# Performance work log

Hardware: AMD Instinct MI355X
Metric: run time of the kernel (lower is better)

Reference implementation:

```python
import jax, jax.numpy as jnp
import numpy as np

NEG_INF = -9e15
LEAKY_SLOPE = 0.01  # PyTorch F.leaky_relu default


def setup_inputs() -> dict:
    key = jax.random.key(0)
    k1, k2, k3, k4 = jax.random.split(key, 4)
    B, N, Fin, Fout = 4, 4096, 64, 64
    X = jax.random.normal(k1, (B, N, Fin), dtype=jnp.float32)
    A = jax.random.randint(k2, (N, N), 0, 2, dtype=jnp.int32)
    weight = jax.random.normal(k3, (Fin, Fout), dtype=jnp.float32) * 0.15
    a = jax.random.normal(k4, (2 * Fout, 1), dtype=jnp.float32) * 0.15
    return {"X": X, "A": A, "weight": weight, "a": a}


def reference(X, A, weight, a):
    B, N, _ = X.shape
    Fout = weight.shape[1]
    # add self loops: A[i,i] = 1
    mask = (A > 0) | jnp.eye(N, dtype=bool)  # [N, N]
    Xw = jnp.matmul(X, weight)  # [B, N, Fout]
    # additive attention: e_ij = leaky_relu(a_l . x_i + a_r . x_j)
    # equivalent to the repeat/cat/matmul in the original, without O(N^2 F) memory
    a_l = a[:Fout, 0]   # [Fout]
    a_r = a[Fout:, 0]   # [Fout]
    left = jnp.einsum('bnf,f->bn', Xw, a_l)   # [B, N]
    right = jnp.einsum('bnf,f->bn', Xw, a_r)  # [B, N]
    e = left[:, :, None] + right[:, None, :]  # [B, N, N]
    e = jnp.where(e >= 0, e, LEAKY_SLOPE * e)
    att = jnp.where(mask[None, :, :], e, NEG_INF)
    att = jax.nn.softmax(att, axis=-1)  # dropout p=0 -> identity
    out = jnp.matmul(att, Xw)  # [B, N, Fout]
    return out
```

## Files before the change

### kernel.cpp

```cpp
#include <hip/hip_runtime.h>
#include <hip/hip_bf16.h>
#include <math.h>

#define BB 4
#define NN 4096
#define FF 64
#define KS (NN / 32)
#define NKW (KS / 4)
#define C0F 3.35462628e-4f
#define C1F 3.35462628e-6f

typedef _Float16 half8 __attribute__((ext_vector_type(8)));
typedef float f32x4 __attribute__((ext_vector_type(4)));

__global__ void k_pack(const int* __restrict__ A, unsigned int* __restrict__ bitsT) {
    int idx = blockIdx.x * 256 + threadIdx.x;
    int row = idx >> 12;
    int col = idx & (NN - 1);
    bool pred = (A[idx] > 0) || (row == col);
    unsigned long long m = __ballot(pred);
    int lane = threadIdx.x & 63;
    if (lane == 0)  bitsT[(size_t)(col >> 5) * NN + row] = (unsigned int)(m & 0xffffffffULL);
    if (lane == 32) bitsT[(size_t)(col >> 5) * NN + row] = (unsigned int)(m >> 32);
}

__global__ __launch_bounds__(256, 2)
void k_pre(const float* __restrict__ X, const float* __restrict__ W,
           const float* __restrict__ avec, _Float16* __restrict__ XwP,
           float2* __restrict__ LE, float2* __restrict__ RE) {
    __shared__ __align__(16) float Wl[64 * 64];
    __shared__ __align__(16) float Xl[32][64];
    __shared__ __align__(16) float T[32][65];
    __shared__ float al[64];
    __shared__ float ar[64];
    const int t = threadIdx.x;
    const int lane = t & 63;
    const int wv = t >> 6;
    const int r0 = blockIdx.x * 32;

    #pragma unroll
    for (int k = 0; k < 16; ++k) Wl[t + k * 256] = W[t + k * 256];
    if (t < 64) { al[t] = avec[t]; ar[t] = avec[64 + t]; }
    {
        const float4* xs = (const float4*)(X + (size_t)r0 * 64);
        float4* xd = (float4*)&Xl[0][0];
        xd[t] = xs[t];
        xd[t + 256] = xs[t + 256];
    }
    __syncthreads();

    float Wreg[64];
    #pragma unroll
    for (int k = 0; k < 64; ++k) Wreg[k] = Wl[k * 64 + lane];

    #pragma unroll
    for (int rr = 0; rr < 8; ++rr) {
        int lrow = wv * 8 + rr;
        int row  = r0 + lrow;
        float a0 = 0.f, a1 = 0.f, a2 = 0.f, a3 = 0.f;
        #pragma unroll
        for (int k = 0; k < 64; k += 4) {
            float4 x = *(const float4*)&Xl[lrow][k];
            a0 = fmaf(x.x, Wreg[k],     a0);
            a1 = fmaf(x.y, Wreg[k + 1], a1);
            a2 = fmaf(x.z, Wreg[k + 2], a2);
            a3 = fmaf(x.w, Wreg[k + 3], a3);
        }
        float acc = (a0 + a1) + (a2 + a3);
        T[lrow][lane] = acc;

        float lv = acc * al[lane];
        float rv = acc * ar[lane];
        #pragma unroll
        for (int off = 32; off; off >>= 1) {
            lv += __shfl_xor(lv, off, 64);
            rv += __shfl_xor(rv, off, 64);
        }
        if (lane == 0) {
            LE[row] = make_float2(lv, __expf(lv - 8.f));
            RE[row] = make_float2(rv, __expf(rv));
        }
    }
    __syncthreads();

    int b  = r0 >> 12;
    int ks = (r0 & (NN - 1)) >> 5;
    int ct = t >> 6;
    int q  = lane >> 4, n = lane & 15;
    half8 h;
    #pragma unroll
    for (int jj = 0; jj < 8; ++jj)
        h[jj] = (_Float16)T[q * 8 + jj][ct * 16 + n];
    *(half8*)&XwP[((((size_t)b * KS + ks) * 4 + ct) * 64 + lane) * 8] = h;
}

__global__ __launch_bounds__(256, 4)
void k_main(const _Float16* __restrict__ XwP, const float2* __restrict__ LE,
            const float2* __restrict__ RE, const unsigned int* __restrict__ bitsT,
            float* __restrict__ out) {
    __shared__ __align__(16) char smem[32768];
    float2* REs = (float2*)smem;
    float (*Lacc)[16][68] = (float (*)[16][68])smem;
    float* Lsum = (float*)(smem + 8704);

    const int t  = threadIdx.x;
    const int b  = blockIdx.y;
    const int i0 = blockIdx.x * 16;

    const int lane = t & 63;
    const int wv   = t >> 6;
    const int lm   = lane & 15;
    const int q    = lane >> 4;

    const int row0 = i0 + lm;
    const float2 le0 = LE[b * NN + row0];
    const _Float16* xp = XwP + (size_t)b * KS * 2048 + (size_t)lane * 8;

    {
        const float4* rsrc = (const float4*)(RE + (size_t)b * NN);
        float4* rdst = (float4*)REs;
        #pragma unroll
        for (int k = 0; k < 8; ++k) rdst[t + k * 256] = rsrc[t + k * 256];
    }
    __syncthreads();

    f32x4 acc[4];
    f32x4 sacc = (f32x4)0.f;
    #pragma unroll
    for (int ct = 0; ct < 4; ++ct) acc[ct] = (f32x4)0.f;
    half8 vones;
    #pragma unroll
    for (int k = 0; k < 8; ++k) vones[k] = (_Float16)1.0f;

    const int ks0 = wv * NKW;

    const _Float16* base = xp + (size_t)ks0 * 2048;
    half8 nb0 = *(const half8*)(base + 0 * 512);
    half8 nb1 = *(const half8*)(base + 1 * 512);
    half8 nb2 = *(const half8*)(base + 2 * 512);
    half8 nb3 = *(const half8*)(base + 3 * 512);
    unsigned int nw0 = bitsT[(size_t)ks0 * NN + row0];

    #pragma unroll 4
    for (int kk = 0; kk < NKW; ++kk) {
        half8 bf0 = nb0, bf1 = nb1, bf2 = nb2, bf3 = nb3;
        unsigned int w0 = nw0 >> (q * 8);

        {
            int nk = kk + 1 < NKW ? kk + 1 : kk;
            const _Float16* nbase = xp + (size_t)(ks0 + nk) * 2048;
            nb0 = *(const half8*)(nbase + 0 * 512);
            nb1 = *(const half8*)(nbase + 1 * 512);
            nb2 = *(const half8*)(nbase + 2 * 512);
            nb3 = *(const half8*)(nbase + 3 * 512);
            nw0 = bitsT[(size_t)(ks0 + nk) * NN + row0];
        }

        const float4* rp = (const float4*)(REs + (ks0 + kk) * 32 + q * 8);
        float4 ra = rp[0], rb = rp[1], rc = rp[2], rd = rp[3];
        float r8[8]  = {ra.x, ra.z, rb.x, rb.z, rc.x, rc.z, rd.x, rd.z};
        float er8[8] = {ra.y, ra.w, rb.y, rb.w, rc.y, rc.w, rd.y, rd.w};

        half8 a0;
        #pragma unroll
        for (int jj = 0; jj < 8; ++jj) {
            float e0 = le0.x + r8[jj];
            float p0 = fmaxf(le0.y * er8[jj], fmaf(e0, C1F, C0F));
            p0 = ((w0 >> jj) & 1u) ? p0 : 0.f;
            a0[jj] = (_Float16)p0;
        }

        acc[0] = __builtin_amdgcn_mfma_f32_16x16x32_f16(a0, bf0, acc[0], 0, 0, 0);
        acc[1] = __builtin_amdgcn_mfma_f32_16x16x32_f16(a0, bf1, acc[1], 0, 0, 0);
        acc[2] = __builtin_amdgcn_mfma_f32_16x16x32_f16(a0, bf2, acc[2], 0, 0, 0);
        acc[3] = __builtin_amdgcn_mfma_f32_16x16x32_f16(a0, bf3, acc[3], 0, 0, 0);
        sacc   = __builtin_amdgcn_mfma_f32_16x16x32_f16(a0, vones, sacc, 0, 0, 0);
    }

    __syncthreads();

    if (wv >= 2) {
        #pragma unroll
        for (int r = 0; r < 4; ++r) {
            int lrow = q * 4 + r;
            #pragma unroll
            for (int ct = 0; ct < 4; ++ct)
                Lacc[wv - 2][lrow][ct * 16 + lm] = acc[ct][r];
            if (lm == 0) Lsum[(wv - 2) * 16 + lrow] = sacc[r];
        }
    }
    __syncthreads();
    if (wv < 2) {
        #pragma unroll
        for (int r = 0; r < 4; ++r) {
            int lrow = q * 4 + r;
            #pragma unroll
            for (int ct = 0; ct < 4; ++ct)
                Lacc[wv][lrow][ct * 16 + lm] += acc[ct][r];
            if (lm == 0) Lsum[wv * 16 + lrow] += sacc[r];
        }
    }
    __syncthreads();
    {
        int lrow = t >> 4;
        int c0   = (t & 15) * 4;
        float s = Lsum[0 * 16 + lrow] + Lsum[1 * 16 + lrow];
        float inv = 1.f / s;
        float4 o;
        o.x = (Lacc[0][lrow][c0 + 0] + Lacc[1][lrow][c0 + 0]) * inv;
        o.y = (Lacc[0][lrow][c0 + 1] + Lacc[1][lrow][c0 + 1]) * inv;
        o.z = (Lacc[0][lrow][c0 + 2] + Lacc[1][lrow][c0 + 2]) * inv;
        o.w = (Lacc[0][lrow][c0 + 3] + Lacc[1][lrow][c0 + 3]) * inv;
        *(float4*)&out[((size_t)(b * NN + i0 + lrow) << 6) + c0] = o;
    }
}

extern "C" void kernel_launch(void* const* d_in, const int* in_sizes, int n_in,
                              void* d_out, int out_size, void* d_ws, size_t ws_size,
                              hipStream_t stream) {
    const float* X    = (const float*)d_in[0];
    const int*   A    = (const int*)d_in[1];
    const float* W    = (const float*)d_in[2];
    const float* avec = (const float*)d_in[3];
    float* out = (float*)d_out;

    char* ws = (char*)d_ws;
    size_t off = 0;
    _Float16* XwP = (_Float16*)(ws + off); off += (size_t)BB * NN * FF * 2;
    float2* LE = (float2*)(ws + off);      off += (size_t)BB * NN * 8;
    float2* RE = (float2*)(ws + off);      off += (size_t)BB * NN * 8;
    unsigned int* bitsT = (unsigned int*)(ws + off);
    off += (size_t)KS * NN * 4;
    (void)off; (void)ws_size;

    k_pack<<<NN * NN / 256, 256, 0, stream>>>(A, bitsT);
    k_pre<<<BB * NN / 32, 256, 0, stream>>>(X, W, avec, XwP, LE, RE);
    k_main<<<dim3(NN / 16, BB), 256, 0, stream>>>(XwP, LE, RE, bitsT, out);
}
```

Baseline: 153.5 us.

## Process two 16-row tiles per block to reuse Xw fragments and RE loads

Each k_main block now handles 32 query rows instead of 16, computing two sets of attention weights and MFMA accumulators against the same loaded Xw fragments and shared RE values. This halves the grid and the global traffic for the XwP value matrix per output row, and it amortizes the RE shared-memory staging. In exchange it raises register pressure, so launch bounds drop to 2 blocks/SM and the unroll to 2, and fewer blocks (512) may leave the GPU less occupied.

Result: faster. 147.4 us (-3.9%).

```diff
diff --git a/kernel.cpp b/kernel.cpp
--- a/kernel.cpp
+++ b/kernel.cpp
@@ -94,26 +94,28 @@
     *(half8*)&XwP[((((size_t)b * KS + ks) * 4 + ct) * 64 + lane) * 8] = h;
 }
 
-__global__ __launch_bounds__(256, 4)
+__global__ __launch_bounds__(256, 2)
 void k_main(const _Float16* __restrict__ XwP, const float2* __restrict__ LE,
             const float2* __restrict__ RE, const unsigned int* __restrict__ bitsT,
             float* __restrict__ out) {
     __shared__ __align__(16) char smem[32768];
     float2* REs = (float2*)smem;
-    float (*Lacc)[16][68] = (float (*)[16][68])smem;
-    float* Lsum = (float*)(smem + 8704);
+    float (*Lacc)[32][68] = (float (*)[32][68])smem;
+    float* Lsum = (float*)(smem + 17408);
 
     const int t  = threadIdx.x;
     const int b  = blockIdx.y;
-    const int i0 = blockIdx.x * 16;
+    const int i0 = blockIdx.x * 32;
 
     const int lane = t & 63;
     const int wv   = t >> 6;
     const int lm   = lane & 15;
     const int q    = lane >> 4;
 
-    const int row0 = i0 + lm;
-    const float2 le0 = LE[b * NN + row0];
+    const int rowa = i0 + lm;
+    const int rowb = i0 + 16 + lm;
+    const float2 lea = LE[b * NN + rowa];
+    const float2 leb = LE[b * NN + rowb];
     const _Float16* xp = XwP + (size_t)b * KS * 2048 + (size_t)lane * 8;
 
     {
@@ -124,10 +126,10 @@
     }
     __syncthreads();
 
-    f32x4 acc[4];
-    f32x4 sacc = (f32x4)0.f;
-    #pragma unroll
-    for (int ct = 0; ct < 4; ++ct) acc[ct] = (f32x4)0.f;
+    f32x4 acca[4], accb[4];
+    f32x4 sacca = (f32x4)0.f, saccb = (f32x4)0.f;
+    #pragma unroll
+    for (int ct = 0; ct < 4; ++ct) { acca[ct] = (f32x4)0.f; accb[ct] = (f32x4)0.f; }
     half8 vones;
     #pragma unroll
     for (int k = 0; k < 8; ++k) vones[k] = (_Float16)1.0f;
@@ -139,12 +141,14 @@
     half8 nb1 = *(const half8*)(base + 1 * 512);
     half8 nb2 = *(const half8*)(base + 2 * 512);
     half8 nb3 = *(const half8*)(base + 3 * 512);
-    unsigned int nw0 = bitsT[(size_t)ks0 * NN + row0];
-
-    #pragma unroll 4
+    unsigned int nwa = bitsT[(size_t)ks0 * NN + rowa];
+    unsigned int nwb = bitsT[(size_t)ks0 * NN + rowb];
+
+    #pragma unroll 2
     for (int kk = 0; kk < NKW; ++kk) {
         half8 bf0 = nb0, bf1 = nb1, bf2 = nb2, bf3 = nb3;
-        unsigned int w0 = nw0 >> (q * 8);
+        unsigned int wa = nwa >> (q * 8);
+        unsigned int wb = nwb >> (q * 8);
 
         {
             int nk = kk + 1 < NKW ? kk + 1 : kk;
@@ -153,7 +157,8 @@
             nb1 = *(const half8*)(nbase + 1 * 512);
             nb2 = *(const half8*)(nbase + 2 * 512);
             nb3 = *(const half8*)(nbase + 3 * 512);
-            nw0 = bitsT[(size_t)(ks0 + nk) * NN + row0];
+            nwa = bitsT[(size_t)(ks0 + nk) * NN + rowa];
+            nwb = bitsT[(size_t)(ks0 + nk) * NN + rowb];
         }
 
         const float4* rp = (const float4*)(REs + (ks0 + kk) * 32 + q * 8);
@@ -161,20 +166,32 @@
         float r8[8]  = {ra.x, ra.z, rb.x, rb.z, rc.x, rc.z, rd.x, rd.z};
         float er8[8] = {ra.y, ra.w, rb.y, rb.w, rc.y, rc.w, rd.y, rd.w};
 
-        half8 a0;
+        half8 a0a, a0b;
         #pragma unroll
         for (int jj = 0; jj < 8; ++jj) {
-            float e0 = le0.x + r8[jj];
-            float p0 = fmaxf(le0.y * er8[jj], fmaf(e0, C1F, C0F));
-            p0 = ((w0 >> jj) & 1u) ? p0 : 0.f;
-            a0[jj] = (_Float16)p0;
-        }
-
-        acc[0] = __builtin_amdgcn_mfma_f32_16x16x32_f16(a0, bf0, acc[0], 0, 0, 0);
-        acc[1] = __builtin_amdgcn_mfma_f32_16x16x32_f16(a0, bf1, acc[1], 0, 0, 0);
-        acc[2] = __builtin_amdgcn_mfma_f32_16x16x32_f16(a0, bf2, acc[2], 0, 0, 0);
-        acc[3] = __builtin_amdgcn_mfma_f32_16x16x32_f16(a0, bf3, acc[3], 0, 0, 0);
-        sacc   = __builtin_amdgcn_mfma_f32_16x16x32_f16(a0, vones, sacc, 0, 0, 0);
+            float e0 = lea.x + r8[jj];
+            float p0 = fmaxf(lea.y * er8[jj], fmaf(e0, C1F, C0F));
+            p0 = ((wa >> jj) & 1u) ? p0 : 0.f;
+            a0a[jj] = (_Float16)p0;
+        }
+        acca[0] = __builtin_amdgcn_mfma_f32_16x16x32_f16(a0a, bf0, acca[0], 0, 0, 0);
+        acca[1] = __builtin_amdgcn_mfma_f32_16x16x32_f16(a0a, bf1, acca[1], 0, 0, 0);
+        acca[2] = __builtin_amdgcn_mfma_f32_16x16x32_f16(a0a, bf2, acca[2], 0, 0, 0);
+        acca[3] = __builtin_amdgcn_mfma_f32_16x16x32_f16(a0a, bf3, acca[3], 0, 0, 0);
+        sacca   = __builtin_amdgcn_mfma_f32_16x16x32_f16(a0a, vones, sacca, 0, 0, 0);
+
+        #pragma unroll
+        for (int jj = 0; jj < 8; ++jj) {
+            float e0 = leb.x + r8[jj];
+            float p0 = fmaxf(leb.y * er8[jj], fmaf(e0, C1F, C0F));
+            p0 = ((wb >> jj) & 1u) ? p0 : 0.f;
+            a0b[jj] = (_Float16)p0;
+        }
+        accb[0] = __builtin_amdgcn_mfma_f32_16x16x32_f16(a0b, bf0, accb[0], 0, 0, 0);
+        accb[1] = __builtin_amdgcn_mfma_f32_16x16x32_f16(a0b, bf1, accb[1], 0, 0, 0);
+        accb[2] = __builtin_amdgcn_mfma_f32_16x16x32_f16(a0b, bf2, accb[2], 0, 0, 0);
+        accb[3] = __builtin_amdgcn_mfma_f32_16x16x32_f16(a0b, bf3, accb[3], 0, 0, 0);
+        saccb   = __builtin_amdgcn_mfma_f32_16x16x32_f16(a0b, vones, saccb, 0, 0, 0);
     }
 
     __syncthreads();
@@ -184,9 +201,14 @@
         for (int r = 0; r < 4; ++r) {
             int lrow = q * 4 + r;
             #pragma unroll
-            for (int ct = 0; ct < 4; ++ct)
-                Lacc[wv - 2][lrow][ct * 16 + lm] = acc[ct][r];
-            if (lm == 0) Lsum[(wv - 2) * 16 + lrow] = sacc[r];
+            for (int ct = 0; ct < 4; ++ct) {
+                Lacc[wv - 2][lrow][ct * 16 + lm]      = acca[ct][r];
+                Lacc[wv - 2][16 + lrow][ct * 16 + lm] = accb[ct][r];
+            }
+            if (lm == 0) {
+                Lsum[(wv - 2) * 32 + lrow]      = sacca[r];
+                Lsum[(wv - 2) * 32 + 16 + lrow] = saccb[r];
+            }
         }
     }
     __syncthreads();
@@ -195,16 +217,23 @@
         for (int r = 0; r < 4; ++r) {
             int lrow = q * 4 + r;
             #pragma unroll
-            for (int ct = 0; ct < 4; ++ct)
-                Lacc[wv][lrow][ct * 16 + lm] += acc[ct][r];
-            if (lm == 0) Lsum[wv * 16 + lrow] += sacc[r];
-        }
-    }
-    __syncthreads();
-    {
-        int lrow = t >> 4;
-        int c0   = (t & 15) * 4;
-        float s = Lsum[0 * 16 + lrow] + Lsum[1 * 16 + lrow];
+            for (int ct = 0; ct < 4; ++ct) {
+                Lacc[wv][lrow][ct * 16 + lm]      += acca[ct][r];
+                Lacc[wv][16 + lrow][ct * 16 + lm] += accb[ct][r];
+            }
+            if (lm == 0) {
+                Lsum[wv * 32 + lrow]      += sacca[r];
+                Lsum[wv * 32 + 16 + lrow] += saccb[r];
+            }
+        }
+    }
+    __syncthreads();
+    #pragma unroll
+    for (int it = 0; it < 2; ++it) {
+        int idx  = t + it * 256;
+        int lrow = idx >> 4;
+        int c0   = (idx & 15) * 4;
+        float s = Lsum[lrow] + Lsum[32 + lrow];
         float inv = 1.f / s;
         float4 o;
         o.x = (Lacc[0][lrow][c0 + 0] + Lacc[1][lrow][c0 + 0]) * inv;
@@ -235,5 +264,5 @@
 
     k_pack<<<NN * NN / 256, 256, 0, stream>>>(A, bitsT);
     k_pre<<<BB * NN / 32, 256, 0, stream>>>(X, W, avec, XwP, LE, RE);
-    k_main<<<dim3(NN / 16, BB), 256, 0, stream>>>(XwP, LE, RE, bitsT, out);
-}
+    k_main<<<dim3(NN / 32, BB), 256, 0, stream>>>(XwP, LE, RE, bitsT, out);
+}
```
